# Kernel optimization log

Measured on AMD Instinct MI355X. Metric: run time of the kernel, lower is better.

## Reference

```python
import jax, jax.numpy as jnp
import numpy as np

N = 50000
E = 600000
D_IN = 128
D_OUT = 128
EPS = 1e-12  # F.normalize eps


def setup_inputs() -> dict:
    key = jax.random.key(0)
    ks = jax.random.split(key, 10)
    s = 1.0 / np.sqrt(D_IN)
    inp = {
        "x": jax.random.normal(ks[0], (N, D_IN), dtype=jnp.float32),
        "edge_index": jax.random.randint(ks[1], (2, E), 0, N, dtype=jnp.int64),
        # conv1: lin_l (with bias) applied to aggregated neighbors, lin_r (no bias) to root
        "W1l": jax.random.uniform(ks[2], (D_IN, D_IN), jnp.float32, -s, s),
        "b1": jax.random.uniform(ks[3], (D_IN,), jnp.float32, -s, s),
        "W1r": jax.random.uniform(ks[4], (D_IN, D_IN), jnp.float32, -s, s),
        # conv2
        "W2l": jax.random.uniform(ks[5], (D_IN, D_OUT), jnp.float32, -s, s),
        "b2": jax.random.uniform(ks[6], (D_OUT,), jnp.float32, -s, s),
        "W2r": jax.random.uniform(ks[7], (D_IN, D_OUT), jnp.float32, -s, s),
        # final fc
        "Wf": jax.random.uniform(ks[8], (D_OUT, D_OUT), jnp.float32, -s, s),
        "bf": jax.random.uniform(ks[9], (D_OUT,), jnp.float32, -s, s),
    }
    return inp


def _sage_conv(x, src, dst, Wl, bl, Wr):
    # mean-aggregate messages from source nodes onto destination nodes
    msgs = x[src]  # [E, d] gather
    agg = jax.ops.segment_sum(msgs, dst, num_segments=N)  # [N, d]
    cnt = jax.ops.segment_sum(jnp.ones((src.shape[0],), x.dtype), dst, num_segments=N)
    agg = agg / jnp.maximum(cnt, 1.0)[:, None]  # isolated nodes -> 0
    out = agg @ Wl + bl + x @ Wr
    # L2 normalize per node (PyG normalize=True)
    nrm = jnp.sqrt(jnp.sum(out * out, axis=-1, keepdims=True))
    return out / jnp.maximum(nrm, EPS)


def reference(x, edge_index, W1l, b1, W1r, W2l, b2, W2r, Wf, bf):
    src, dst = edge_index[0], edge_index[1]
    h = jax.nn.relu(_sage_conv(x, src, dst, W1l, b1, W1r))
    h = jax.nn.relu(_sage_conv(h, src, dst, W2l, b2, W2r))
    return h @ Wf + bf
```

## Files before the change

### kernel.cpp

```cpp
#include <hip/hip_runtime.h>
#include <hip/hip_fp16.h>

#define D 128
#define SCAN_B 256

typedef __attribute__((ext_vector_type(8))) _Float16 f16x8;
typedef __attribute__((ext_vector_type(4))) float f32x4;

typedef __attribute__((address_space(1))) const void gas_t;
typedef __attribute__((address_space(3))) void las_t;

__global__ void scan_pass1(const int* __restrict__ cnt, int* __restrict__ rs,
                           int* __restrict__ bsum, int N) {
    __shared__ int lds[SCAN_B];
    int tid = threadIdx.x;
    int i = blockIdx.x * SCAN_B + tid;
    int v = (i < N) ? cnt[i] : 0;
    lds[tid] = v;
    __syncthreads();
    for (int o = 1; o < SCAN_B; o <<= 1) {
        int t = (tid >= o) ? lds[tid - o] : 0;
        __syncthreads();
        lds[tid] += t;
        __syncthreads();
    }
    if (i < N) rs[i] = lds[tid] - v;
    if (tid == SCAN_B - 1) bsum[blockIdx.x] = lds[tid];
}

__global__ void scan_pass2(int* __restrict__ bsum, int nb) {
    __shared__ int lds[SCAN_B];
    int tid = threadIdx.x;
    int v = (tid < nb) ? bsum[tid] : 0;
    lds[tid] = v;
    __syncthreads();
    for (int o = 1; o < SCAN_B; o <<= 1) {
        int t = (tid >= o) ? lds[tid - o] : 0;
        __syncthreads();
        lds[tid] += t;
        __syncthreads();
    }
    if (tid < nb) bsum[tid] = lds[tid] - v;
}

__global__ void scan_pass3(int* __restrict__ rs, int* __restrict__ cursor,
                           const int* __restrict__ bsum, const int* __restrict__ cnt,
                           float* __restrict__ inv, int N) {
    int i = blockIdx.x * SCAN_B + threadIdx.x;
    if (i < N) {
        int v = rs[i] + bsum[blockIdx.x];
        rs[i] = v;
        cursor[i] = v;
        inv[i] = 1.0f / (float)max(cnt[i], 1);
    }
}

__global__ void fill_kernel(const int* __restrict__ ei, int E,
                            int* __restrict__ cursor, int* __restrict__ csr) {
    int e = blockIdx.x * blockDim.x + threadIdx.x;
    if (e < E) {
        int src = ei[e], dst = ei[E + e];
        int pos = atomicAdd(&cursor[dst], 1);
        csr[pos] = src;
    }
}

__global__ void prologue_kernel(const float* __restrict__ W1l, const float* __restrict__ W1r,
                                const float* __restrict__ W2l, const float* __restrict__ W2r,
                                const float* __restrict__ Wf, unsigned short* __restrict__ pw,
                                const float* __restrict__ x, __half* __restrict__ xh,
                                __half* __restrict__ xl, int n8,
                                const int* __restrict__ ei, int E, int* __restrict__ cnt) {
    int t = blockIdx.x * blockDim.x + threadIdx.x;
    if (t < 10240) {
        int idx = t;
        int w = idx >> 11;
        int r = idx & 2047;
        int ks = r >> 9;
        int tt = (r >> 6) & 7;
        int lane = r & 63;
        int q = lane >> 4, n = lane & 15;
        const float* W = (w == 0) ? W1l : (w == 1) ? W1r : (w == 2) ? W2l : (w == 3) ? W2r : Wf;
        unsigned short* dh = pw + (size_t)w * 32768;
        unsigned short* dl = dh + 16384;
        int off = ((ks * 8 + tt) * 64 + lane) * 8;
#pragma unroll
        for (int j = 0; j < 8; j++) {
            float v = W[(size_t)(ks * 32 + q * 8 + j) * D + tt * 16 + n];
            __half hb = __float2half_rn(v);
            dh[off + j] = __half_as_ushort(hb);
            dl[off + j] = __half_as_ushort(__float2half_rn(v - __half2float(hb)));
        }
    } else if (t < 10240 + n8) {
        int i = t - 10240;
        const float4* x4 = (const float4*)x;
        float4 a = x4[2 * i], b = x4[2 * i + 1];
        float v[8] = {a.x, a.y, a.z, a.w, b.x, b.y, b.z, b.w};
        uint4 oh, ol;
        __half2* ph = (__half2*)&oh;
        __half2* pl = (__half2*)&ol;
#pragma unroll
        for (int jj = 0; jj < 4; jj++) {
            __half h0 = __float2half_rn(v[2 * jj]);
            __half h1 = __float2half_rn(v[2 * jj + 1]);
            ph[jj] = __halves2half2(h0, h1);
            pl[jj] = __halves2half2(__float2half_rn(v[2 * jj] - __half2float(h0)),
                                    __float2half_rn(v[2 * jj + 1] - __half2float(h1)));
        }
        ((uint4*)xh)[i] = oh;
        ((uint4*)xl)[i] = ol;
    } else {
        int e = t - 10240 - n8;
        if (e < E) atomicAdd(&cnt[ei[E + e]], 1);
    }
}

__device__ __forceinline__ void acc8(uint4 v, float* s) {
    const __half2* h = reinterpret_cast<const __half2*>(&v);
    float2 f0 = __half22float2(h[0]);
    float2 f1 = __half22float2(h[1]);
    float2 f2 = __half22float2(h[2]);
    float2 f3 = __half22float2(h[3]);
    s[0] += f0.x; s[1] += f0.y; s[2] += f1.x; s[3] += f1.y;
    s[4] += f2.x; s[5] += f2.y; s[6] += f3.x; s[7] += f3.y;
}

__device__ __forceinline__ void split_f16(const float* v, uint4& hi, uint4& lo) {
    __half2* ph = (__half2*)&hi;
    __half2* pl = (__half2*)&lo;
#pragma unroll
    for (int jj = 0; jj < 4; jj++) {
        __half h0 = __float2half_rn(v[2 * jj]);
        __half h1 = __float2half_rn(v[2 * jj + 1]);
        ph[jj] = __halves2half2(h0, h1);
        pl[jj] = __halves2half2(__float2half_rn(v[2 * jj] - __half2float(h0)),
                                __float2half_rn(v[2 * jj + 1] - __half2float(h1)));
    }
}

template <int LAYER>
__global__ __launch_bounds__(256) void fused_gemm(
        const int* __restrict__ csr, const int* __restrict__ rs,
        const int* __restrict__ cnt, const float* __restrict__ inv,
        const uint4* __restrict__ Gsrc,
        const uint4* __restrict__ Ah1, const uint4* __restrict__ Al1,
        const uint4* __restrict__ W0h, const uint4* __restrict__ W0l,
        const uint4* __restrict__ W1h, const uint4* __restrict__ W1l,
        const float* __restrict__ bias,
        const uint4* __restrict__ W2h, const uint4* __restrict__ W2l,
        const float* __restrict__ bias2,
        float* out, __half* Hout, int N) {
    __shared__ uint4 smem4[2048];
    const int GS = (LAYER == 1) ? 16 : 32;

    const int tid = threadIdx.x;
    const int lane = tid & 63;
    const int wave = tid >> 6;
    const int c = lane & 15;
    const int q = lane >> 4;
    const int R = blockIdx.x * 64 + wave * 16;
    const int row0 = min(R + c, N - 1);
    const size_t rbA1 = (size_t)row0 * GS + q;

#define STAGE_W(ks_, b_)                                                                   \
    do {                                                                                   \
        const uint4* sh_ = (((ks_) < 4) ? W0h : W1h) + (size_t)((ks_) & 3) * 512;          \
        const uint4* sl_ = (((ks_) < 4) ? W0l : W1l) + (size_t)((ks_) & 3) * 512;          \
        const uint4* s_ = ((wave < 2) ? sh_ : sl_) + ((wave & 1) * 256 + lane);            \
        uint4* d_ = smem4 + (b_) * 1024 + (wave >> 1) * 512 + (wave & 1) * 256;            \
        __builtin_amdgcn_global_load_lds((gas_t*)(s_), (las_t*)(d_), 16, 0, 0);            \
        __builtin_amdgcn_global_load_lds((gas_t*)(s_ + 64), (las_t*)(d_ + 64), 16, 0, 0);  \
        __builtin_amdgcn_global_load_lds((gas_t*)(s_ + 128), (las_t*)(d_ + 128), 16, 0, 0);\
        __builtin_amdgcn_global_load_lds((gas_t*)(s_ + 192), (las_t*)(d_ + 192), 16, 0, 0);\
    } while (0)

    STAGE_W(0, 0);
    STAGE_W(1, 1);
    uint4 Xs_h[4], Xs_l[4];
#pragma unroll
    for (int kl = 0; kl < 4; kl++) {
        Xs_h[kl] = Ah1[rbA1 + kl * 4];
        Xs_l[kl] = Al1[rbA1 + kl * 4];
    }

    int deg = cnt[row0];
    int st = rs[row0];
    float iv = inv[row0];
    float s[4][8];
#pragma unroll
    for (int ks = 0; ks < 4; ks++)
#pragma unroll
        for (int j = 0; j < 8; j++) s[ks][j] = 0.0f;

    int i = 0;
    for (; i + 2 <= deg; i += 2) {
        int n0 = csr[st + i], n1 = csr[st + i + 1];
        const uint4* g0 = Gsrc + (size_t)n0 * GS + q;
        const uint4* g1 = Gsrc + (size_t)n1 * GS + q;
        uint4 a0 = g0[0], a1 = g0[4], a2 = g0[8], a3 = g0[12];
        uint4 b0 = g1[0], b1 = g1[4], b2 = g1[8], b3 = g1[12];
        acc8(a0, s[0]); acc8(a1, s[1]); acc8(a2, s[2]); acc8(a3, s[3]);
        acc8(b0, s[0]); acc8(b1, s[1]); acc8(b2, s[2]); acc8(b3, s[3]);
    }
    if (i < deg) {
        int n0 = csr[st + i];
        const uint4* g0 = Gsrc + (size_t)n0 * GS + q;
        uint4 a0 = g0[0], a1 = g0[4], a2 = g0[8], a3 = g0[12];
        acc8(a0, s[0]); acc8(a1, s[1]); acc8(a2, s[2]); acc8(a3, s[3]);
    }

    uint4 Agg_h[4], Agg_l[4];
#pragma unroll
    for (int ks = 0; ks < 4; ks++) {
        float v[8];
#pragma unroll
        for (int j = 0; j < 8; j++) v[j] = s[ks][j] * iv;
        split_f16(v, Agg_h[ks], Agg_l[ks]);
    }

    asm volatile("s_waitcnt vmcnt(0)" ::: "memory");
    __syncthreads();

    f32x4 acc[8];
#pragma unroll
    for (int t = 0; t < 8; t++)
#pragma unroll
        for (int r = 0; r < 4; r++) acc[t][r] = 0.0f;

#pragma unroll
    for (int ks = 0; ks < 8; ks++) {
        const int b = ks & 1;
        const uint4* wb = smem4 + b * 1024;
        f16x8 ah = __builtin_bit_cast(f16x8, (ks < 4) ? Agg_h[ks & 3] : Xs_h[ks & 3]);
        f16x8 al = __builtin_bit_cast(f16x8, (ks < 4) ? Agg_l[ks & 3] : Xs_l[ks & 3]);
#pragma unroll
        for (int t = 0; t < 8; t++) {
            f16x8 bh = __builtin_bit_cast(f16x8, wb[t * 64 + lane]);
            f16x8 bl = __builtin_bit_cast(f16x8, wb[512 + t * 64 + lane]);
            acc[t] = __builtin_amdgcn_mfma_f32_16x16x32_f16(ah, bh, acc[t], 0, 0, 0);
            acc[t] = __builtin_amdgcn_mfma_f32_16x16x32_f16(al, bh, acc[t], 0, 0, 0);
            acc[t] = __builtin_amdgcn_mfma_f32_16x16x32_f16(ah, bl, acc[t], 0, 0, 0);
        }
        if (ks < 7) {
            asm volatile("s_waitcnt vmcnt(0)" ::: "memory");
            __syncthreads();
            if (ks < 6) STAGE_W(ks + 2, b);
        }
    }

#pragma unroll
    for (int t = 0; t < 8; t++) {
        float bv = bias[t * 16 + c];
#pragma unroll
        for (int r = 0; r < 4; r++) acc[t][r] += bv;
    }
#pragma unroll
    for (int r = 0; r < 4; r++) {
        float v = 0.0f;
#pragma unroll
        for (int t = 0; t < 8; t++) v += acc[t][r] * acc[t][r];
        v += __shfl_xor(v, 1, 16);
        v += __shfl_xor(v, 2, 16);
        v += __shfl_xor(v, 4, 16);
        v += __shfl_xor(v, 8, 16);
        float rn = 1.0f / fmaxf(sqrtf(v), 1e-12f);
#pragma unroll
        for (int t = 0; t < 8; t++) acc[t][r] = fmaxf(acc[t][r] * rn, 0.0f);
    }

    if (LAYER == 1) {
#pragma unroll
        for (int t = 0; t < 8; t++)
#pragma unroll
            for (int r = 0; r < 4; r++) {
                int row = R + q * 4 + r;
                if (row < N) {
                    float v = acc[t][r];
                    __half h = __float2half_rn(v);
                    size_t base = (size_t)row * 256;
                    Hout[base + t * 16 + c] = h;
                    Hout[base + 128 + t * 16 + c] = __float2half_rn(v - __half2float(h));
                }
            }
        return;
    }

    __syncthreads();
    unsigned short* hw = (unsigned short*)(smem4 + wave * 512);
#pragma unroll
    for (int t = 0; t < 8; t++)
#pragma unroll
        for (int r = 0; r < 4; r++) {
            int m = q * 4 + r;
            float v = acc[t][r];
            __half h = __float2half_rn(v);
            int j4 = (t * 2 + (c >> 3)) ^ (m & 7);
            int off = m * 128 + j4 * 8 + (c & 7);
            hw[off] = __half_as_ushort(h);
            hw[2048 + off] = __half_as_ushort(__float2half_rn(v - __half2float(h)));
        }
    uint4 a2h_[4], a2l_[4];
#pragma unroll
    for (int k2 = 0; k2 < 4; k2++) {
        int r4 = (k2 * 4 + q) ^ (c & 7);
        a2h_[k2] = *(const uint4*)(hw + c * 128 + r4 * 8);
        a2l_[k2] = *(const uint4*)(hw + 2048 + c * 128 + r4 * 8);
    }

    f32x4 acc2[8];
#pragma unroll
    for (int t = 0; t < 8; t++) {
        float bv = bias2[t * 16 + c];
#pragma unroll
        for (int r = 0; r < 4; r++) acc2[t][r] = bv;
    }
#pragma unroll
    for (int k2 = 0; k2 < 4; k2++) {
        const uint4* Wh = W2h + (size_t)k2 * 512 + lane;
        const uint4* Wl = W2l + (size_t)k2 * 512 + lane;
        f16x8 ah = __builtin_bit_cast(f16x8, a2h_[k2]);
        f16x8 al = __builtin_bit_cast(f16x8, a2l_[k2]);
#pragma unroll
        for (int t = 0; t < 8; t++) {
            f16x8 bh = __builtin_bit_cast(f16x8, Wh[t * 64]);
            f16x8 bl = __builtin_bit_cast(f16x8, Wl[t * 64]);
            acc2[t] = __builtin_amdgcn_mfma_f32_16x16x32_f16(ah, bh, acc2[t], 0, 0, 0);
            acc2[t] = __builtin_amdgcn_mfma_f32_16x16x32_f16(al, bh, acc2[t], 0, 0, 0);
            acc2[t] = __builtin_amdgcn_mfma_f32_16x16x32_f16(ah, bl, acc2[t], 0, 0, 0);
        }
    }

#pragma unroll
    for (int t = 0; t < 8; t++)
#pragma unroll
        for (int r = 0; r < 4; r++) {
            int row = R + q * 4 + r;
            if (row < N) out[(size_t)row * D + t * 16 + c] = acc2[t][r];
        }
#undef STAGE_W
}

extern "C" void kernel_launch(void* const* d_in, const int* in_sizes, int n_in,
                              void* d_out, int out_size, void* d_ws, size_t ws_size,
                              hipStream_t stream) {
    const float* x   = (const float*)d_in[0];
    const int*   ei  = (const int*)d_in[1];
    const float* W1l = (const float*)d_in[2];
    const float* b1  = (const float*)d_in[3];
    const float* W1r = (const float*)d_in[4];
    const float* W2l = (const float*)d_in[5];
    const float* b2  = (const float*)d_in[6];
    const float* W2r = (const float*)d_in[7];
    const float* Wf  = (const float*)d_in[8];
    const float* bf  = (const float*)d_in[9];
    float* out = (float*)d_out;

    int N = in_sizes[0] / D;
    int E = in_sizes[1] / 2;

    __half* Xh  = (__half*)d_ws;
    __half* Xl  = Xh + (size_t)N * D;
    __half* H1  = Xl + (size_t)N * D;
    float* inv  = (float*)(H1 + (size_t)N * 256);
    int*   rs     = (int*)(inv + N);
    int*   cnt    = rs + N;
    int*   cursor = cnt + N;
    int*   bsum   = cursor + N;
    int*   csr    = bsum + 256;
    unsigned short* pw = (unsigned short*)(csr + E);
    unsigned short* p1lh = pw + 0 * 32768, *p1ll = p1lh + 16384;
    unsigned short* p1rh = pw + 1 * 32768, *p1rl = p1rh + 16384;
    unsigned short* p2lh = pw + 2 * 32768, *p2ll = p2lh + 16384;
    unsigned short* p2rh = pw + 3 * 32768, *p2rl = p2rh + 16384;
    unsigned short* pfh  = pw + 4 * 32768, *pfl  = pfh + 16384;

    int nb = (N + SCAN_B - 1) / SCAN_B;
    int n8 = N * 16;

    hipMemsetAsync(cnt, 0, (size_t)N * sizeof(int), stream);
    int pro_threads = 10240 + n8 + E;
    prologue_kernel<<<(pro_threads + 255) / 256, 256, 0, stream>>>(
        W1l, W1r, W2l, W2r, Wf, pw, x, Xh, Xl, n8, ei, E, cnt);
    scan_pass1<<<nb, SCAN_B, 0, stream>>>(cnt, rs, bsum, N);
    scan_pass2<<<1, SCAN_B, 0, stream>>>(bsum, nb);
    scan_pass3<<<nb, SCAN_B, 0, stream>>>(rs, cursor, bsum, cnt, inv, N);
    fill_kernel<<<(E + 255) / 256, 256, 0, stream>>>(ei, E, cursor, csr);

    int gemm_blocks = (N + 63) / 64;

    fused_gemm<1><<<gemm_blocks, 256, 0, stream>>>(
        csr, rs, cnt, inv,
        (const uint4*)Xh, (const uint4*)Xh, (const uint4*)Xl,
        (const uint4*)p1lh, (const uint4*)p1ll, (const uint4*)p1rh, (const uint4*)p1rl, b1,
        nullptr, nullptr, nullptr, nullptr, H1, N);

    fused_gemm<2><<<gemm_blocks, 256, 0, stream>>>(
        csr, rs, cnt, inv,
        (const uint4*)H1, (const uint4*)H1, (const uint4*)H1 + 16,
        (const uint4*)p2lh, (const uint4*)p2ll, (const uint4*)p2rh, (const uint4*)p2rl, b2,
        (const uint4*)pfh, (const uint4*)pfl, bf, out, nullptr, N);
}
```

Baseline: 271.8 us.

## Restructure neighbor gather so each 16-lane group handles four rows, exchanging via LDS

The mean-aggregation gather now assigns each group of 16 lanes to one destination row at a time. Each lane loads one 16-byte chunk per neighbor, so a whole 256-byte row is read contiguously, with a 4-way unrolled neighbor loop. The aggregated rows are split to fp16 hi/lo, written to LDS with an XOR swizzle, then read back in the MFMA operand layout. The aim is more coalesced gathers and more loads in flight per row, at the cost of extra LDS traffic and barriers. Weight staging into LDS is moved after the gather because the gather reuses the same shared buffer, and a barrier is added before the second-layer LDS readback.

```diff
diff --git a/kernel.cpp b/kernel.cpp
--- a/kernel.cpp
+++ b/kernel.cpp
@@ -174,8 +174,6 @@
         __builtin_amdgcn_global_load_lds((gas_t*)(s_ + 192), (las_t*)(d_ + 192), 16, 0, 0);\
     } while (0)
 
-    STAGE_W(0, 0);
-    STAGE_W(1, 1);
     uint4 Xs_h[4], Xs_l[4];
 #pragma unroll
     for (int kl = 0; kl < 4; kl++) {
@@ -183,41 +181,56 @@
         Xs_l[kl] = Al1[rbA1 + kl * 4];
     }
 
-    int deg = cnt[row0];
-    int st = rs[row0];
-    float iv = inv[row0];
-    float s[4][8];
-#pragma unroll
-    for (int ks = 0; ks < 4; ks++)
-#pragma unroll
-        for (int j = 0; j < 8; j++) s[ks][j] = 0.0f;
-
-    int i = 0;
-    for (; i + 2 <= deg; i += 2) {
-        int n0 = csr[st + i], n1 = csr[st + i + 1];
-        const uint4* g0 = Gsrc + (size_t)n0 * GS + q;
-        const uint4* g1 = Gsrc + (size_t)n1 * GS + q;
-        uint4 a0 = g0[0], a1 = g0[4], a2 = g0[8], a3 = g0[12];
-        uint4 b0 = g1[0], b1 = g1[4], b2 = g1[8], b3 = g1[12];
-        acc8(a0, s[0]); acc8(a1, s[1]); acc8(a2, s[2]); acc8(a3, s[3]);
-        acc8(b0, s[0]); acc8(b1, s[1]); acc8(b2, s[2]); acc8(b3, s[3]);
-    }
-    if (i < deg) {
-        int n0 = csr[st + i];
-        const uint4* g0 = Gsrc + (size_t)n0 * GS + q;
-        uint4 a0 = g0[0], a1 = g0[4], a2 = g0[8], a3 = g0[12];
-        acc8(a0, s[0]); acc8(a1, s[1]); acc8(a2, s[2]); acc8(a3, s[3]);
-    }
+    uint4* aw = smem4 + wave * 512;
+    {
+        const int g = lane >> 4;
+        const int cg = lane & 15;
+#pragma unroll
+        for (int rr = 0; rr < 4; rr++) {
+            int rl = g * 4 + rr;
+            int node = min(R + rl, N - 1);
+            int deg = cnt[node];
+            int st = rs[node];
+            float iv = inv[node];
+            float s[8] = {0.f, 0.f, 0.f, 0.f, 0.f, 0.f, 0.f, 0.f};
+            int i = 0;
+            for (; i + 4 <= deg; i += 4) {
+                int n0 = csr[st + i + 0], n1 = csr[st + i + 1];
+                int n2 = csr[st + i + 2], n3 = csr[st + i + 3];
+                uint4 v0 = Gsrc[(size_t)n0 * GS + cg];
+                uint4 v1 = Gsrc[(size_t)n1 * GS + cg];
+                uint4 v2 = Gsrc[(size_t)n2 * GS + cg];
+                uint4 v3 = Gsrc[(size_t)n3 * GS + cg];
+                acc8(v0, s); acc8(v1, s); acc8(v2, s); acc8(v3, s);
+            }
+            for (; i < deg; i++) {
+                int n0 = csr[st + i];
+                uint4 v0 = Gsrc[(size_t)n0 * GS + cg];
+                acc8(v0, s);
+            }
+            float v[8];
+#pragma unroll
+            for (int j = 0; j < 8; j++) v[j] = s[j] * iv;
+            uint4 hi, lo;
+            split_f16(v, hi, lo);
+            int sidx = rl * 32 + (cg ^ (rl & 7));
+            aw[sidx] = hi;
+            aw[sidx + 16] = lo;
+        }
+    }
+    __syncthreads();
 
     uint4 Agg_h[4], Agg_l[4];
 #pragma unroll
     for (int ks = 0; ks < 4; ks++) {
-        float v[8];
-#pragma unroll
-        for (int j = 0; j < 8; j++) v[j] = s[ks][j] * iv;
-        split_f16(v, Agg_h[ks], Agg_l[ks]);
-    }
-
+        int ridx = c * 32 + ((ks * 4 + q) ^ (c & 7));
+        Agg_h[ks] = aw[ridx];
+        Agg_l[ks] = aw[ridx + 16];
+    }
+    __syncthreads();
+
+    STAGE_W(0, 0);
+    STAGE_W(1, 1);
     asm volatile("s_waitcnt vmcnt(0)" ::: "memory");
     __syncthreads();
 
@@ -299,6 +312,7 @@
             hw[off] = __half_as_ushort(h);
             hw[2048 + off] = __half_as_ushort(__float2half_rn(v - __half2float(h)));
         }
+    __syncthreads();
     uint4 a2h_[4], a2l_[4];
 #pragma unroll
     for (int k2 = 0; k2 < 4; k2++) {
```

Result: slower. 278.0 us (+2.3%).
